# Kernel optimization log

Hardware: AMD Instinct MI355X
Metric: run time of the kernel (lower is better)

The kernel has to match this reference:

```python
import jax, jax.numpy as jnp
import numpy as np
from jax import lax

ACT_SCALE = (0.5, 0.5, 0.5)  # act_scale[0..2], also used as bias_scale
STRIDE = 2
QLEVELS = 127.0  # int8 fake-quant levels (2**7 - 1)


@jax.custom_vjp
def ste_round(x):
    return jnp.round(x)

def _ste_fwd(x):
    return jnp.round(x), None

def _ste_bwd(_, g):
    return (g,)

ste_round.defvjp(_ste_fwd, _ste_bwd)


def fq_act(x, scale):
    # quantize_activations_gemm_A: normalize by scale, clip to [-1,1], 8-bit grid
    return ste_round(jnp.clip(x / scale, -1.0, 1.0) * QLEVELS) / QLEVELS


def qw(w):
    # quantize_weight_gemm_S: per-tensor max-abs scale + 8-bit fake quant
    s = jnp.max(jnp.abs(w))
    wq = ste_round(jnp.clip(w / s, -1.0, 1.0) * QLEVELS) / QLEVELS
    return wq, s


def qb(b):
    # quantize_bias_gemm: round to 1/127 grid
    return ste_round(b * QLEVELS) / QLEVELS


def relu6s(x, scale):
    # ReLU6S: scaled ReLU6
    return jnp.clip(x / scale, 0.0, 6.0)


def conv(x, w, stride=1, pad=0):
    return lax.conv_general_dilated(
        x, w, (stride, stride), [(pad, pad), (pad, pad)],
        dimension_numbers=("NCHW", "OIHW", "NCHW"))


def bottleneck_fwd(x, w1, b1, w2, b2, w3, b3, ws, bs):
    s0, s1, s2a = ACT_SCALE
    x = fq_act(x, s0)
    residual = x
    # conv1: 1x1
    w1q, c1s = qw(w1)
    b1q = qb(b1) / (c1s * s0)
    out = (conv(x, w1q) + b1q[None, :, None, None]) * c1s
    out = relu6s(out, s0) * s0
    out = fq_act(out, s1)
    # conv2: 3x3 stride
    w2q, c2s = qw(w2)
    b2q = qb(b2) / (c2s * s1)
    out = (conv(out, w2q, stride=STRIDE, pad=1) + b2q[None, :, None, None]) * c2s
    out = relu6s(out, s1) * s1
    out = fq_act(out, s2a)
    # conv3: 1x1 (source's padding=1 on a 1x1 conv is a shape bug; dropped)
    w3q, c3s = qw(w3)
    b3q = qb(b3) / (c2s * s2a)  # NOTE: source divides by conv2_scale (preserved)
    out = (conv(out, w3q) + b3q[None, :, None, None]) * c3s
    out = out * s2a
    # downsample shortcut: 1x1 stride
    wsq, css = qw(ws)
    bsq = qb(bs) / (css * s0)
    residual = (conv(residual, wsq, stride=STRIDE) + bsq[None, :, None, None]) * css
    residual = residual * s0
    return jnp.clip(out + residual, 0.0, 6.0)  # final ReLU6


def setup_inputs() -> dict:
    key = jax.random.key(0)
    ks = jax.random.split(key, 9)
    B, Cin, P, H, W = 64, 512, 256, 28, 28
    Cout = 4 * P
    def w_init(k, shape):
        fan_in = shape[1] * shape[2] * shape[3]
        return jax.random.normal(k, shape, jnp.float32) * np.float32(np.sqrt(2.0 / fan_in))
    return {
        "x": jax.random.normal(ks[0], (B, Cin, H, W), jnp.float32),
        "w1": w_init(ks[1], (P, Cin, 1, 1)),
        "b1": jax.random.normal(ks[2], (P,), jnp.float32) * 0.01,
        "w2": w_init(ks[3], (P, P, 3, 3)),
        "b2": jax.random.normal(ks[4], (P,), jnp.float32) * 0.01,
        "w3": w_init(ks[5], (Cout, P, 1, 1)),
        "b3": jax.random.normal(ks[6], (Cout,), jnp.float32) * 0.01,
        "ws": w_init(ks[7], (Cout, Cin, 1, 1)),
        "bs": jax.random.normal(ks[8], (Cout,), jnp.float32) * 0.01,
    }


def reference(x, w1, b1, w2, b2, w3, b3, ws, bs):
    return bottleneck_fwd(x, w1, b1, w2, b2, w3, b3, ws, bs)
```

## Files before the change

### kernel.cpp

```cpp
#include <hip/hip_runtime.h>
#include <stdint.h>

typedef int   int4v __attribute__((ext_vector_type(4)));
typedef float f32x4 __attribute__((ext_vector_type(4)));

#define WS_SCALES 0ull
#define WS_ZERO   256ull
#define WS_BI1    1024ull
#define WS_BI2    2048ull
#define WS_BI3    4096ull
#define WS_BIS    8192ull
#define WS_W1Q    16384ull
#define WS_W2Q    (WS_W1Q + 131072ull)
#define WS_W3Q    (WS_W2Q + 589824ull)
#define WS_WSQ    (WS_W3Q + 262144ull)
#define WS_A0     2097152ull
#define WS_A1     (WS_A0 + 25690112ull)
#define WS_A2     (WS_A1 + 12845056ull)

__device__ __forceinline__ void gll16(const void* g, void* l) {
    __builtin_amdgcn_global_load_lds((const __attribute__((address_space(1))) void*)g,
                                     (__attribute__((address_space(3))) void*)l, 16, 0, 0);
}

__global__ void k_init(float* wshead) {
    int i = blockIdx.x * 256 + threadIdx.x;
    wshead[i] = 0.0f;
}

__global__ void k_maxabs(const float* __restrict__ w1, const float* __restrict__ w2,
                         const float* __restrict__ w3, const float* __restrict__ wsd,
                         float* __restrict__ scales) {
    const float* srcs[4] = {w1, w2, w3, wsd};
    const int ns[4] = {131072, 589824, 262144, 524288};
    int t = blockIdx.y;
    const float* s = srcs[t];
    int n = ns[t];
    float m = 0.0f;
    for (int i = blockIdx.x * 256 + threadIdx.x; i < n; i += gridDim.x * 256)
        m = fmaxf(m, fabsf(s[i]));
    __shared__ float red[256];
    red[threadIdx.x] = m;
    __syncthreads();
    for (int st = 128; st > 0; st >>= 1) {
        if (threadIdx.x < st) red[threadIdx.x] = fmaxf(red[threadIdx.x], red[threadIdx.x + st]);
        __syncthreads();
    }
    if (threadIdx.x == 0) atomicMax((int*)&scales[t], __float_as_int(red[0]));
}

__global__ void k_quant_w(const float* __restrict__ w1, const float* __restrict__ w2,
                          const float* __restrict__ w3, const float* __restrict__ wsd,
                          const float* __restrict__ b1, const float* __restrict__ b2,
                          const float* __restrict__ b3, const float* __restrict__ bs,
                          char* __restrict__ wsb) {
    const float* sc = (const float*)(wsb + WS_SCALES);
    int mode = blockIdx.y;
    int i0 = blockIdx.x * 256 + threadIdx.x;
    int stride = gridDim.x * 256;
    if (mode == 0) {
        float s = sc[0]; signed char* o = (signed char*)(wsb + WS_W1Q);
        for (int i = i0; i < 131072; i += stride)
            o[i] = (signed char)(int)rintf(fminf(fmaxf(w1[i] / s, -1.f), 1.f) * 127.f);
    } else if (mode == 1) {
        float s = sc[1]; signed char* o = (signed char*)(wsb + WS_W2Q);
        for (int i = i0; i < 589824; i += stride) {
            int oo = i / 2304, r2 = i - oo * 2304;
            int c = r2 / 9, kk = r2 - c * 9;
            o[(size_t)oo * 2304 + kk * 256 + c] =
                (signed char)(int)rintf(fminf(fmaxf(w2[i] / s, -1.f), 1.f) * 127.f);
        }
    } else if (mode == 2) {
        float s = sc[2]; signed char* o = (signed char*)(wsb + WS_W3Q);
        for (int i = i0; i < 262144; i += stride)
            o[i] = (signed char)(int)rintf(fminf(fmaxf(w3[i] / s, -1.f), 1.f) * 127.f);
    } else if (mode == 3) {
        float s = sc[3]; signed char* o = (signed char*)(wsb + WS_WSQ);
        for (int i = i0; i < 524288; i += stride)
            o[i] = (signed char)(int)rintf(fminf(fmaxf(wsd[i] / s, -1.f), 1.f) * 127.f);
    } else if (mode == 4) {
        float* o = (float*)(wsb + WS_BI1);
        for (int i = i0; i < 256; i += stride) o[i] = rintf(b1[i] * 127.f);
    } else if (mode == 5) {
        float* o = (float*)(wsb + WS_BI2);
        for (int i = i0; i < 256; i += stride) o[i] = rintf(b2[i] * 127.f);
    } else if (mode == 6) {
        float* o = (float*)(wsb + WS_BI3);
        for (int i = i0; i < 1024; i += stride) o[i] = rintf(b3[i] * 127.f);
    } else {
        float* o = (float*)(wsb + WS_BIS);
        for (int i = i0; i < 1024; i += stride) o[i] = rintf(bs[i] * 127.f);
    }
}

__global__ void k_quant_x(const float* __restrict__ x, signed char* __restrict__ a0) {
    __shared__ signed char tile[32][33];
    int b = blockIdx.z;
    int p0 = blockIdx.x * 32, c0 = blockIdx.y * 32;
    int tp = threadIdx.x & 31, tr = threadIdx.x >> 5;
    const float* xb = x + ((size_t)b * 512 + c0) * 784 + p0;
    for (int i = 0; i < 4; i++) {
        int cc = tr + i * 8;
        float v = (p0 + tp < 784) ? xb[(size_t)cc * 784 + tp] : 0.f;
        v = fminf(fmaxf(v * 2.f, -1.f), 1.f);
        tile[cc][tp] = (signed char)(int)rintf(v * 127.f);
    }
    __syncthreads();
    int pp = threadIdx.x >> 3, cs = (threadIdx.x & 7) * 4;
    if (p0 + pp < 784) {
        unsigned pk = 0;
        for (int i = 0; i < 4; i++)
            pk |= (unsigned)(unsigned char)tile[cs + i][pp] << (8 * i);
        *(unsigned*)(a0 + ((size_t)b * 784 + p0 + pp) * 512 + c0 + cs) = pk;
    }
}

template <int MODE, int BM, int BN, int WGM, int WGN>
__global__ __launch_bounds__(256) void k_conv(char* __restrict__ wsb, float* __restrict__ dout) {
    constexpr int FM = BM / WGM / 16;
    constexpr int FN = BN / WGN / 16;
    constexpr int ISS_A = BM / 16;
    constexpr int NISS = (BM + BN) / 16;
    constexpr int NI = NISS / 4;
    constexpr int KTOT = (MODE == 0) ? 512 : (MODE == 1) ? 2304 : 768;
    constexpr int NSTEP = KTOT / 64;
    constexpr int BMP = BM + 16;
    constexpr int LDS_STAGE = (BM + BN) * 64;
    constexpr int LDS_EPI = (MODE == 2) ? 64 * (BN + 4) * 4 : BN * BMP;
    constexpr int LDSZ = (2 * LDS_STAGE > LDS_EPI) ? 2 * LDS_STAGE : LDS_EPI;

    __shared__ alignas(16) char lds[LDSZ];

    const int tid = threadIdx.x;
    const int wid = tid >> 6;
    const int lane = tid & 63;
    const int n0 = blockIdx.x * BN;
    const int m0 = blockIdx.y * BM;
    const int bb = blockIdx.z;

    const float* sc = (const float*)(wsb + WS_SCALES);
    const int srow = lane >> 2;
    const int lrow = lane & 15;
    const int quad = lane >> 4;
    const int wm = (wid % WGM) * (BM / WGM);
    const int wn = (wid / WGM) * (BN / WGN);
    const int xco = ((lane & 3) ^ ((lane >> 3) & 3)) << 4;
    const char* zp = wsb + WS_ZERO + xco;

    int4v acc3[FM][FN] = {};
    int4v accS[FM][FN] = {};

    auto src_ptr = [&](int s, int k0) -> const char* {
        const char* g;
        if (s < ISS_A) {
            int m = m0 + s * 16 + srow;
            if (MODE == 0)
                g = wsb + WS_W1Q + (size_t)m * 512 + k0 + xco;
            else if (MODE == 1)
                g = wsb + WS_W2Q + (size_t)m * 2304 + k0 + xco;
            else
                g = (k0 < 256) ? wsb + WS_W3Q + (size_t)m * 256 + k0 + xco
                               : wsb + WS_WSQ + (size_t)m * 512 + (k0 - 256) + xco;
        } else {
            int n = n0 + (s - ISS_A) * 16 + srow;
            g = zp;
            if (MODE == 0) {
                g = wsb + WS_A0 + (size_t)n * 512 + k0 + xco;
            } else if (MODE == 1) {
                unsigned b = (unsigned)n / 196u;
                unsigned hw = (unsigned)n - b * 196u;
                int oh = hw / 14, ow = hw - oh * 14;
                int tap = k0 >> 8;
                int kh = tap / 3, kw = tap - kh * 3;
                int c0 = k0 & 255;
                int ih = 2 * oh - 1 + kh, iw = 2 * ow - 1 + kw;
                if (ih >= 0 && ih < 28 && iw >= 0 && iw < 28)
                    g = wsb + WS_A1 + ((size_t)b * 784 + ih * 28 + iw) * 256 + c0 + xco;
            } else {
                if (n < 196) {
                    if (k0 < 256) {
                        g = wsb + WS_A2 + ((size_t)bb * 196 + n) * 256 + k0 + xco;
                    } else {
                        int oh = n / 14, ow = n - oh * 14;
                        int ps = oh * 56 + ow * 2;
                        g = wsb + WS_A0 + ((size_t)bb * 784 + ps) * 512 + (k0 - 256) + xco;
                    }
                }
            }
        }
        return g;
    };

    auto stage = [&](int t, char* buf) {
        const int k0 = t * 64;
#pragma unroll
        for (int ii = 0; ii < NI; ii++) {
            const int s = wid + ii * 4;
            gll16(src_ptr(s, k0), buf + s * 1024);
        }
    };

    stage(0, lds);
    for (int t = 0; t < NSTEP; ++t) {
        char* cur = lds + (t & 1) * LDS_STAGE;
        char* nxt = lds + ((t & 1) ^ 1) * LDS_STAGE;
        __syncthreads();
        if (t + 1 < NSTEP) stage(t + 1, nxt);

        int4v afr[FM], bfr[FN];
#pragma unroll
        for (int i = 0; i < FM; i++) {
            int m = wm + i * 16 + lrow;
            afr[i] = *(const int4v*)(cur + m * 64 + ((quad ^ ((m >> 1) & 3)) << 4));
        }
#pragma unroll
        for (int j = 0; j < FN; j++) {
            int n = wn + j * 16 + lrow;
            bfr[j] = *(const int4v*)(cur + (BM + n) * 64 + ((quad ^ ((n >> 1) & 3)) << 4));
        }
        if (MODE != 2 || t < 4) {
#pragma unroll
            for (int i = 0; i < FM; i++)
#pragma unroll
                for (int j = 0; j < FN; j++)
                    acc3[i][j] = __builtin_amdgcn_mfma_i32_16x16x64_i8(afr[i], bfr[j], acc3[i][j], 0, 0, 0);
        } else {
#pragma unroll
            for (int i = 0; i < FM; i++)
#pragma unroll
                for (int j = 0; j < FN; j++)
                    accS[i][j] = __builtin_amdgcn_mfma_i32_16x16x64_i8(afr[i], bfr[j], accS[i][j], 0, 0, 0);
        }
    }

    if (MODE == 0 || MODE == 1) {
        const float alpha = sc[MODE] / 16129.0f;
        const float* bi = (const float*)(wsb + (MODE == 0 ? WS_BI1 : WS_BI2));
        signed char* outp = (signed char*)(wsb + (MODE == 0 ? WS_A1 : WS_A2));
        __syncthreads();
#pragma unroll
        for (int i = 0; i < FM; i++) {
            int mloc = wm + i * 16 + quad * 4;
            int mb = m0 + mloc;
            float bt[4];
#pragma unroll
            for (int r = 0; r < 4; r++) bt[r] = bi[mb + r] * (2.0f / 127.0f);
#pragma unroll
            for (int j = 0; j < FN; j++) {
                int nloc = wn + j * 16 + lrow;
                unsigned pk = 0;
#pragma unroll
                for (int r = 0; r < 4; r++) {
                    float v = alpha * (float)acc3[i][j][r] + bt[r];
                    int q = (int)rintf(127.0f * fminf(fmaxf(2.0f * v, 0.0f), 1.0f));
                    pk |= (unsigned)(q & 0xFF) << (8 * r);
                }
                *(unsigned*)(lds + nloc * BMP + mloc) = pk;
            }
        }
        __syncthreads();
        for (int u = tid; u < BN * (BM / 16); u += 256) {
            int row = u / (BM / 16);
            int seg = u % (BM / 16);
            uint4 v = *(const uint4*)(lds + row * BMP + seg * 16);
            *(uint4*)(outp + (size_t)(n0 + row) * 256 + m0 + seg * 16) = v;
        }
    } else {
        const float c2 = sc[1], c3 = sc[2], cS = sc[3];
        const float* bi3 = (const float*)(wsb + WS_BI3);
        const float* bis = (const float*)(wsb + WS_BIS);
        float* ldsF = (float*)lds;
        constexpr int LDN = BN + 4;
        constexpr int SEGS = BN / 16;
        for (int half = 0; half < 2; half++) {
            __syncthreads();
            if (wm == half * 64) {
#pragma unroll
                for (int i = 0; i < FM; i++) {
                    int mloc = i * 16 + quad * 4;
                    int mg = m0 + half * 64 + mloc;
                    float bt[4];
#pragma unroll
                    for (int r = 0; r < 4; r++)
                        bt[r] = bi3[mg + r] * (c3 / (127.0f * c2)) + bis[mg + r] * (1.0f / 127.0f);
#pragma unroll
                    for (int j = 0; j < FN; j++) {
                        int nloc = wn + j * 16 + lrow;
#pragma unroll
                        for (int r = 0; r < 4; r++) {
                            float v = (c3 * (float)acc3[i][j][r] + cS * (float)accS[i][j][r])
                                          * (0.5f / 16129.0f) + bt[r];
                            v = v < 0.0f ? 0.0f : (v > 6.0f ? 6.0f : v);
                            ldsF[(mloc + r) * LDN + nloc] = v;
                        }
                    }
                }
            }
            __syncthreads();
            {
                int rw0 = tid / SEGS, seg = tid % SEGS;
                int nbase = n0 + seg * 16;
                for (int row = rw0; row < 64; row += 256 / SEGS) {
                    const float* src = ldsF + row * LDN + seg * 16;
                    float* dst = dout + ((size_t)bb * 1024 + m0 + half * 64 + row) * 196 + nbase;
                    if (nbase + 16 <= 196) {
                        *(f32x4*)(dst + 0)  = *(const f32x4*)(src + 0);
                        *(f32x4*)(dst + 4)  = *(const f32x4*)(src + 4);
                        *(f32x4*)(dst + 8)  = *(const f32x4*)(src + 8);
                        *(f32x4*)(dst + 12) = *(const f32x4*)(src + 12);
                    } else {
                        for (int q = 0; q < 16 && nbase + q < 196; q++) dst[q] = src[q];
                    }
                }
            }
        }
    }
}

extern "C" void kernel_launch(void* const* d_in, const int* in_sizes, int n_in,
                              void* d_out, int out_size, void* d_ws, size_t ws_size,
                              hipStream_t stream) {
    const float* x   = (const float*)d_in[0];
    const float* w1  = (const float*)d_in[1];
    const float* b1  = (const float*)d_in[2];
    const float* w2  = (const float*)d_in[3];
    const float* b2  = (const float*)d_in[4];
    const float* w3  = (const float*)d_in[5];
    const float* b3  = (const float*)d_in[6];
    const float* wsd = (const float*)d_in[7];
    const float* bs  = (const float*)d_in[8];
    float* out = (float*)d_out;
    char* wsb = (char*)d_ws;

    k_init<<<16, 256, 0, stream>>>((float*)wsb);
    k_maxabs<<<dim3(32, 4), 256, 0, stream>>>(w1, w2, w3, wsd, (float*)(wsb + WS_SCALES));
    k_quant_w<<<dim3(96, 8), 256, 0, stream>>>(w1, w2, w3, wsd, b1, b2, b3, bs, wsb);
    k_quant_x<<<dim3(25, 16, 64), 256, 0, stream>>>(x, (signed char*)(wsb + WS_A0));
    k_conv<0, 128, 128, 2, 2><<<dim3(392, 2, 1), 256, 0, stream>>>(wsb, out);
    k_conv<1, 64, 128, 2, 2><<<dim3(98, 4, 1), 256, 0, stream>>>(wsb, out);
    k_conv<2, 128, 128, 2, 2><<<dim3(2, 8, 64), 256, 0, stream>>>(wsb, out);
}
```

Baseline: 341.2 us.

## Load MFMA fragments directly from global memory instead of LDS staging

Removes the global_load_lds double-buffered LDS staging in the conv GEMM kernels. Each lane now loads its int8 MFMA fragments straight from global memory into registers, with a two-deep software prefetch and precomputed per-lane base pointers. The per-step __syncthreads calls go away and LDS is used only for the epilogue. Tile shapes shrink to BM=64 and launch_bounds min-waves hints are added to raise occupancy. The cost is that rows are no longer shared through LDS, so each wave fetches its own data: global and L2 traffic rises and there is more per-lane address arithmetic.

```diff
diff --git a/kernel.cpp b/kernel.cpp
--- a/kernel.cpp
+++ b/kernel.cpp
@@ -17,11 +17,6 @@
 #define WS_A0     2097152ull
 #define WS_A1     (WS_A0 + 25690112ull)
 #define WS_A2     (WS_A1 + 12845056ull)
-
-__device__ __forceinline__ void gll16(const void* g, void* l) {
-    __builtin_amdgcn_global_load_lds((const __attribute__((address_space(1))) void*)g,
-                                     (__attribute__((address_space(3))) void*)l, 16, 0, 0);
-}
 
 __global__ void k_init(float* wshead) {
     int i = blockIdx.x * 256 + threadIdx.x;
@@ -115,19 +110,14 @@
     }
 }
 
-template <int MODE, int BM, int BN, int WGM, int WGN>
-__global__ __launch_bounds__(256) void k_conv(char* __restrict__ wsb, float* __restrict__ dout) {
+template <int MODE, int BM, int BN, int WGM, int WGN, int MINW>
+__global__ __launch_bounds__(256, MINW) void k_conv(char* __restrict__ wsb, float* __restrict__ dout) {
     constexpr int FM = BM / WGM / 16;
     constexpr int FN = BN / WGN / 16;
-    constexpr int ISS_A = BM / 16;
-    constexpr int NISS = (BM + BN) / 16;
-    constexpr int NI = NISS / 4;
     constexpr int KTOT = (MODE == 0) ? 512 : (MODE == 1) ? 2304 : 768;
     constexpr int NSTEP = KTOT / 64;
     constexpr int BMP = BM + 16;
-    constexpr int LDS_STAGE = (BM + BN) * 64;
-    constexpr int LDS_EPI = (MODE == 2) ? 64 * (BN + 4) * 4 : BN * BMP;
-    constexpr int LDSZ = (2 * LDS_STAGE > LDS_EPI) ? 2 * LDS_STAGE : LDS_EPI;
+    constexpr int LDSZ = (MODE == 2) ? BM * (BN + 4) * 4 : BN * BMP;
 
     __shared__ alignas(16) char lds[LDSZ];
 
@@ -139,105 +129,113 @@
     const int bb = blockIdx.z;
 
     const float* sc = (const float*)(wsb + WS_SCALES);
-    const int srow = lane >> 2;
     const int lrow = lane & 15;
     const int quad = lane >> 4;
     const int wm = (wid % WGM) * (BM / WGM);
     const int wn = (wid / WGM) * (BN / WGN);
-    const int xco = ((lane & 3) ^ ((lane >> 3) & 3)) << 4;
-    const char* zp = wsb + WS_ZERO + xco;
+    const char* zpq = wsb + WS_ZERO + quad * 16;
+
+    const char* aB[FM];
+    const char* aB2[FM];
+    const char* bB[FN];
+    const char* bB2[FN];
+    int oh2[FN], ow2[FN];
+
+#pragma unroll
+    for (int i = 0; i < FM; i++) {
+        int m = m0 + wm + i * 16 + lrow;
+        if constexpr (MODE == 0) {
+            aB[i] = wsb + WS_W1Q + (size_t)m * 512 + quad * 16;
+        } else if constexpr (MODE == 1) {
+            aB[i] = wsb + WS_W2Q + (size_t)m * 2304 + quad * 16;
+        } else {
+            aB[i]  = wsb + WS_W3Q + (size_t)m * 256 + quad * 16;
+            aB2[i] = wsb + WS_WSQ + (size_t)m * 512 + quad * 16;
+        }
+    }
+#pragma unroll
+    for (int j = 0; j < FN; j++) {
+        int n = n0 + wn + j * 16 + lrow;
+        if constexpr (MODE == 0) {
+            bB[j] = wsb + WS_A0 + (size_t)n * 512 + quad * 16;
+        } else if constexpr (MODE == 1) {
+            unsigned b = (unsigned)n / 196u;
+            unsigned hw = (unsigned)n - b * 196u;
+            int oh = hw / 14, ow = hw - oh * 14;
+            bB[j] = wsb + WS_A1 + (size_t)b * 200704 + quad * 16;
+            oh2[j] = 2 * oh - 1;
+            ow2[j] = 2 * ow - 1;
+        } else {
+            if (n < 196) {
+                int oh = n / 14, ow = n - oh * 14;
+                bB[j]  = wsb + WS_A2 + ((size_t)bb * 196 + n) * 256 + quad * 16;
+                bB2[j] = wsb + WS_A0 + ((size_t)bb * 784 + oh * 56 + ow * 2) * 512 + quad * 16;
+            } else {
+                bB[j] = zpq; bB2[j] = zpq;
+            }
+        }
+    }
 
     int4v acc3[FM][FN] = {};
     int4v accS[FM][FN] = {};
 
-    auto src_ptr = [&](int s, int k0) -> const char* {
-        const char* g;
-        if (s < ISS_A) {
-            int m = m0 + s * 16 + srow;
-            if (MODE == 0)
-                g = wsb + WS_W1Q + (size_t)m * 512 + k0 + xco;
-            else if (MODE == 1)
-                g = wsb + WS_W2Q + (size_t)m * 2304 + k0 + xco;
-            else
-                g = (k0 < 256) ? wsb + WS_W3Q + (size_t)m * 256 + k0 + xco
-                               : wsb + WS_WSQ + (size_t)m * 512 + (k0 - 256) + xco;
+    auto loadF = [&](int t, int4v (&a)[FM], int4v (&b)[FN]) {
+        if constexpr (MODE == 0) {
+            const int off = t * 64;
+#pragma unroll
+            for (int i = 0; i < FM; i++) a[i] = *(const int4v*)(aB[i] + off);
+#pragma unroll
+            for (int j = 0; j < FN; j++) b[j] = *(const int4v*)(bB[j] + off);
+        } else if constexpr (MODE == 1) {
+            const int off = t * 64;
+#pragma unroll
+            for (int i = 0; i < FM; i++) a[i] = *(const int4v*)(aB[i] + off);
+            const int tap = t >> 2, c0 = (t & 3) << 6;
+            const int kh = tap / 3, kw = tap - 3 * kh;
+#pragma unroll
+            for (int j = 0; j < FN; j++) {
+                int ih = oh2[j] + kh, iw = ow2[j] + kw;
+                const char* g = ((unsigned)ih < 28u && (unsigned)iw < 28u)
+                                    ? bB[j] + (ih * 28 + iw) * 256 + c0 : zpq;
+                b[j] = *(const int4v*)g;
+            }
         } else {
-            int n = n0 + (s - ISS_A) * 16 + srow;
-            g = zp;
-            if (MODE == 0) {
-                g = wsb + WS_A0 + (size_t)n * 512 + k0 + xco;
-            } else if (MODE == 1) {
-                unsigned b = (unsigned)n / 196u;
-                unsigned hw = (unsigned)n - b * 196u;
-                int oh = hw / 14, ow = hw - oh * 14;
-                int tap = k0 >> 8;
-                int kh = tap / 3, kw = tap - kh * 3;
-                int c0 = k0 & 255;
-                int ih = 2 * oh - 1 + kh, iw = 2 * ow - 1 + kw;
-                if (ih >= 0 && ih < 28 && iw >= 0 && iw < 28)
-                    g = wsb + WS_A1 + ((size_t)b * 784 + ih * 28 + iw) * 256 + c0 + xco;
+            if (t < 4) {
+                const int off = t * 64;
+#pragma unroll
+                for (int i = 0; i < FM; i++) a[i] = *(const int4v*)(aB[i] + off);
+#pragma unroll
+                for (int j = 0; j < FN; j++) b[j] = *(const int4v*)(bB[j] + off);
             } else {
-                if (n < 196) {
-                    if (k0 < 256) {
-                        g = wsb + WS_A2 + ((size_t)bb * 196 + n) * 256 + k0 + xco;
-                    } else {
-                        int oh = n / 14, ow = n - oh * 14;
-                        int ps = oh * 56 + ow * 2;
-                        g = wsb + WS_A0 + ((size_t)bb * 784 + ps) * 512 + (k0 - 256) + xco;
-                    }
-                }
-            }
-        }
-        return g;
+                const int off = (t - 4) * 64;
+#pragma unroll
+                for (int i = 0; i < FM; i++) a[i] = *(const int4v*)(aB2[i] + off);
+#pragma unroll
+                for (int j = 0; j < FN; j++) b[j] = *(const int4v*)(bB2[j] + off);
+            }
+        }
     };
-
-    auto stage = [&](int t, char* buf) {
-        const int k0 = t * 64;
-#pragma unroll
-        for (int ii = 0; ii < NI; ii++) {
-            const int s = wid + ii * 4;
-            gll16(src_ptr(s, k0), buf + s * 1024);
-        }
+    auto MF = [&](int4v (&ac)[FM][FN], int4v (&a)[FM], int4v (&b)[FN]) {
+#pragma unroll
+        for (int i = 0; i < FM; i++)
+#pragma unroll
+            for (int j = 0; j < FN; j++)
+                ac[i][j] = __builtin_amdgcn_mfma_i32_16x16x64_i8(a[i], b[j], ac[i][j], 0, 0, 0);
     };
 
-    stage(0, lds);
-    for (int t = 0; t < NSTEP; ++t) {
-        char* cur = lds + (t & 1) * LDS_STAGE;
-        char* nxt = lds + ((t & 1) ^ 1) * LDS_STAGE;
-        __syncthreads();
-        if (t + 1 < NSTEP) stage(t + 1, nxt);
-
-        int4v afr[FM], bfr[FN];
-#pragma unroll
-        for (int i = 0; i < FM; i++) {
-            int m = wm + i * 16 + lrow;
-            afr[i] = *(const int4v*)(cur + m * 64 + ((quad ^ ((m >> 1) & 3)) << 4));
-        }
-#pragma unroll
-        for (int j = 0; j < FN; j++) {
-            int n = wn + j * 16 + lrow;
-            bfr[j] = *(const int4v*)(cur + (BM + n) * 64 + ((quad ^ ((n >> 1) & 3)) << 4));
-        }
-        if (MODE != 2 || t < 4) {
-#pragma unroll
-            for (int i = 0; i < FM; i++)
-#pragma unroll
-                for (int j = 0; j < FN; j++)
-                    acc3[i][j] = __builtin_amdgcn_mfma_i32_16x16x64_i8(afr[i], bfr[j], acc3[i][j], 0, 0, 0);
-        } else {
-#pragma unroll
-            for (int i = 0; i < FM; i++)
-#pragma unroll
-                for (int j = 0; j < FN; j++)
-                    accS[i][j] = __builtin_amdgcn_mfma_i32_16x16x64_i8(afr[i], bfr[j], accS[i][j], 0, 0, 0);
-        }
-    }
-
-    if (MODE == 0 || MODE == 1) {
+    int4v aC[FM], bC[FN], aN[FM], bN[FN];
+    loadF(0, aC, bC);
+    for (int t = 0; t < NSTEP; t += 2) {
+        loadF(t + 1, aN, bN);
+        if (MODE != 2 || t < 4) MF(acc3, aC, bC); else MF(accS, aC, bC);
+        if (t + 2 < NSTEP) loadF(t + 2, aC, bC);
+        if (MODE != 2 || t + 1 < 4) MF(acc3, aN, bN); else MF(accS, aN, bN);
+    }
+
+    if constexpr (MODE == 0 || MODE == 1) {
         const float alpha = sc[MODE] / 16129.0f;
         const float* bi = (const float*)(wsb + (MODE == 0 ? WS_BI1 : WS_BI2));
         signed char* outp = (signed char*)(wsb + (MODE == 0 ? WS_A1 : WS_A2));
-        __syncthreads();
 #pragma unroll
         for (int i = 0; i < FM; i++) {
             int mloc = wm + i * 16 + quad * 4;
@@ -272,45 +270,40 @@
         float* ldsF = (float*)lds;
         constexpr int LDN = BN + 4;
         constexpr int SEGS = BN / 16;
-        for (int half = 0; half < 2; half++) {
-            __syncthreads();
-            if (wm == half * 64) {
-#pragma unroll
-                for (int i = 0; i < FM; i++) {
-                    int mloc = i * 16 + quad * 4;
-                    int mg = m0 + half * 64 + mloc;
-                    float bt[4];
-#pragma unroll
-                    for (int r = 0; r < 4; r++)
-                        bt[r] = bi3[mg + r] * (c3 / (127.0f * c2)) + bis[mg + r] * (1.0f / 127.0f);
-#pragma unroll
-                    for (int j = 0; j < FN; j++) {
-                        int nloc = wn + j * 16 + lrow;
-#pragma unroll
-                        for (int r = 0; r < 4; r++) {
-                            float v = (c3 * (float)acc3[i][j][r] + cS * (float)accS[i][j][r])
-                                          * (0.5f / 16129.0f) + bt[r];
-                            v = v < 0.0f ? 0.0f : (v > 6.0f ? 6.0f : v);
-                            ldsF[(mloc + r) * LDN + nloc] = v;
-                        }
-                    }
+#pragma unroll
+        for (int i = 0; i < FM; i++) {
+            int mloc = i * 16 + quad * 4;
+            int mg = m0 + mloc;
+            float bt[4];
+#pragma unroll
+            for (int r = 0; r < 4; r++)
+                bt[r] = bi3[mg + r] * (c3 / (127.0f * c2)) + bis[mg + r] * (1.0f / 127.0f);
+#pragma unroll
+            for (int j = 0; j < FN; j++) {
+                int nloc = wn + j * 16 + lrow;
+#pragma unroll
+                for (int r = 0; r < 4; r++) {
+                    float v = (c3 * (float)acc3[i][j][r] + cS * (float)accS[i][j][r])
+                                  * (0.5f / 16129.0f) + bt[r];
+                    v = v < 0.0f ? 0.0f : (v > 6.0f ? 6.0f : v);
+                    ldsF[(mloc + r) * LDN + nloc] = v;
                 }
             }
-            __syncthreads();
-            {
-                int rw0 = tid / SEGS, seg = tid % SEGS;
-                int nbase = n0 + seg * 16;
-                for (int row = rw0; row < 64; row += 256 / SEGS) {
-                    const float* src = ldsF + row * LDN + seg * 16;
-                    float* dst = dout + ((size_t)bb * 1024 + m0 + half * 64 + row) * 196 + nbase;
-                    if (nbase + 16 <= 196) {
-                        *(f32x4*)(dst + 0)  = *(const f32x4*)(src + 0);
-                        *(f32x4*)(dst + 4)  = *(const f32x4*)(src + 4);
-                        *(f32x4*)(dst + 8)  = *(const f32x4*)(src + 8);
-                        *(f32x4*)(dst + 12) = *(const f32x4*)(src + 12);
-                    } else {
-                        for (int q = 0; q < 16 && nbase + q < 196; q++) dst[q] = src[q];
-                    }
+        }
+        __syncthreads();
+        {
+            int rw0 = tid / SEGS, seg = tid % SEGS;
+            int nbase = n0 + seg * 16;
+            for (int row = rw0; row < BM; row += 256 / SEGS) {
+                const float* src = ldsF + row * LDN + seg * 16;
+                float* dst = dout + ((size_t)bb * 1024 + m0 + row) * 196 + nbase;
+                if (nbase + 16 <= 196) {
+                    *(f32x4*)(dst + 0)  = *(const f32x4*)(src + 0);
+                    *(f32x4*)(dst + 4)  = *(const f32x4*)(src + 4);
+                    *(f32x4*)(dst + 8)  = *(const f32x4*)(src + 8);
+                    *(f32x4*)(dst + 12) = *(const f32x4*)(src + 12);
+                } else {
+                    for (int q = 0; q < 16 && nbase + q < 196; q++) dst[q] = src[q];
                 }
             }
         }
@@ -336,7 +329,7 @@
     k_maxabs<<<dim3(32, 4), 256, 0, stream>>>(w1, w2, w3, wsd, (float*)(wsb + WS_SCALES));
     k_quant_w<<<dim3(96, 8), 256, 0, stream>>>(w1, w2, w3, wsd, b1, b2, b3, bs, wsb);
     k_quant_x<<<dim3(25, 16, 64), 256, 0, stream>>>(x, (signed char*)(wsb + WS_A0));
-    k_conv<0, 128, 128, 2, 2><<<dim3(392, 2, 1), 256, 0, stream>>>(wsb, out);
-    k_conv<1, 64, 128, 2, 2><<<dim3(98, 4, 1), 256, 0, stream>>>(wsb, out);
-    k_conv<2, 128, 128, 2, 2><<<dim3(2, 8, 64), 256, 0, stream>>>(wsb, out);
-}
+    k_conv<0, 64, 128, 2, 2, 4><<<dim3(392, 4, 1), 256, 0, stream>>>(wsb, out);
+    k_conv<1, 64, 128, 2, 2, 3><<<dim3(98, 4, 1), 256, 0, stream>>>(wsb, out);
+    k_conv<2, 64, 128, 1, 4, 3><<<dim3(2, 16, 64), 256, 0, stream>>>(wsb, out);
+}
```

Result: slower. 410.9 us (+20.4%).
